# Kernel optimization log

Hardware: AMD Instinct MI355X
Metric: run time of the kernel (lower is better)

## Reference

```python
import jax, jax.numpy as jnp
import numpy as np

B, L, D = 4, 2048, 1024
MD = D // 4      # memory_dim = dim // 4
K = 5            # kernel_size
DIL = 1          # dilation
EPS = 1e-6


def rmsnorm(x, w):
    return w * x * jax.lax.rsqrt(jnp.mean(x * x, axis=-1, keepdims=True) + EPS)


def setup_inputs() -> dict:
    key = jax.random.key(0)
    ks = jax.random.split(key, 16)
    n = lambda k, shape, s=0.02: jax.random.normal(k, shape, jnp.float32) * s
    return dict(
        x=jax.random.normal(ks[0], (B, L, D), jnp.float32),
        memory_state=jnp.zeros((B, MD), jnp.float32),
        norm_w=jnp.ones((D,), jnp.float32),
        dw_kernel=n(ks[1], (D, 1, K), 0.1),   # depthwise conv [O,I/g,K]
        dw_bias=jnp.zeros((D,), jnp.float32),
        pw_kernel=n(ks[2], (D, D)),           # 1x1 conv as [out,in]
        pw_bias=jnp.zeros((D,), jnp.float32),
        Win_w=n(ks[3], (MD, D)), Win_b=jnp.zeros((MD,), jnp.float32),
        Wf_w=n(ks[4], (MD, D + MD)), Wf_b=jnp.ones((MD,), jnp.float32),  # forget bias init 1.0
        Wu_w=n(ks[5], (MD, D + MD)), Wu_b=jnp.zeros((MD,), jnp.float32),
        Wo_w=n(ks[6], (D, D + MD)), Wo_b=jnp.zeros((D,), jnp.float32),
        router_w=n(ks[7], (2, D)), router_b=jnp.zeros((2,), jnp.float32),
        e0_w1=n(ks[8], (D, D)), e0_b1=jnp.zeros((D,), jnp.float32),
        e0_w2=n(ks[9], (D, D)), e0_b2=jnp.zeros((D,), jnp.float32),
        e1_w1=n(ks[10], (D, D)), e1_b1=jnp.zeros((D,), jnp.float32),
        e1_w2=n(ks[11], (D, D)), e1_b2=jnp.zeros((D,), jnp.float32),
        fnorm_w=jnp.ones((D,), jnp.float32),
        down_w=n(ks[12], (D // 4, D)), down_b=jnp.zeros((D // 4,), jnp.float32),
        up_w=n(ks[13], (D, D // 4)), up_b=jnp.zeros((D,), jnp.float32),
    )


def reference(x, memory_state, norm_w, dw_kernel, dw_bias, pw_kernel, pw_bias,
              Win_w, Win_b, Wf_w, Wf_b, Wu_w, Wu_b, Wo_w, Wo_b,
              router_w, router_b, e0_w1, e0_b1, e0_w2, e0_b2,
              e1_w1, e1_b1, e1_w2, e1_b2, fnorm_w, down_w, down_b, up_w, up_b):
    resid = x
    xn = rmsnorm(x, norm_w)                              # [B,L,D]

    # --- causal depthwise conv (left pad (K-1)*DIL == torch pad-both + slice[:L]) + pointwise ---
    P = (K - 1) * DIL
    xc = jnp.swapaxes(xn, 1, 2)                          # [B,D,L]
    xc = jax.lax.conv_general_dilated(
        xc, dw_kernel, window_strides=(1,), padding=[(P, 0)],
        rhs_dilation=(DIL,), dimension_numbers=('NCH', 'OIH', 'NCH'),
        feature_group_count=D) + dw_bias[None, :, None]
    x_conv = jnp.einsum('bdl,ed->ble', xc, pw_kernel) + pw_bias  # [B,L,D]

    # --- structured state recurrence (gated, scan over time) ---
    Wf_x, Wf_m = Wf_w[:, :D], Wf_w[:, D:]
    Wu_x, Wu_m = Wu_w[:, :D], Wu_w[:, D:]
    Wo_x, Wo_m = Wo_w[:, :D], Wo_w[:, D:]
    # precompute all x-dependent projections: [L,B,*]
    fx = jnp.einsum('bld,md->lbm', xn, Wf_x) + Wf_b
    ux = jnp.einsum('bld,md->lbm', xn, Wu_x) + Wu_b
    ox = jnp.einsum('bld,ed->lbe', xn, Wo_x) + Wo_b
    xm = jax.nn.silu(jnp.einsum('bld,md->lbm', xn, Win_w) + Win_b)
    xt = jnp.swapaxes(xn, 0, 1)                          # [L,B,D]

    def step(m, inp):
        fx_t, ux_t, ox_t, xm_t, x_t = inp
        f = jax.nn.sigmoid(fx_t + m @ Wf_m.T)
        u = jax.nn.sigmoid(ux_t + m @ Wu_m.T)
        m2 = f * m + u * xm_t
        out = x_t + ox_t + m2 @ Wo_m.T
        return m2, out

    new_mem, rec = jax.lax.scan(step, memory_state, (fx, ux, ox, xm, xt))
    x_rec = jnp.swapaxes(rec, 0, 1)                      # [B,L,D]

    y = x_conv + x_rec

    # --- enhanced gated fusion (2-expert soft MoE) ---
    r = jax.nn.softmax(y @ router_w.T + router_b, axis=-1)   # [B,L,2]
    e0 = jax.nn.silu(y @ e0_w1.T + e0_b1) @ e0_w2.T + e0_b2
    e1 = jax.nn.silu(y @ e1_w1.T + e1_b1) @ e1_w2.T + e1_b2
    y = rmsnorm(y + r[..., 0:1] * e0 + r[..., 1:2] * e1, fnorm_w)

    # --- low-rank FF (exact GELU) + residual ---
    ff = jax.nn.gelu(y @ down_w.T + down_b, approximate=False) @ up_w.T + up_b
    out = y + ff + resid
    return out, new_mem
```

## Files before the change

kernel.cpp:

```cpp
#include <hip/hip_runtime.h>
#include <hip/hip_bf16.h>

#define DD 1024
#define MDD 256
#define LL 2048
#define BB 4
#define NROWS (BB*LL)

typedef short bf16x8 __attribute__((ext_vector_type(8)));
typedef float f32x4 __attribute__((ext_vector_type(4)));

__device__ __forceinline__ short f2b(float x){
  __hip_bfloat16 h = __float2bfloat16(x);
  return *reinterpret_cast<short*>(&h);
}
__device__ __forceinline__ float b2f(short s){
  return __uint_as_float(((unsigned)(unsigned short)s) << 16);
}
__device__ __forceinline__ float frcp(float x){
#if __has_builtin(__builtin_amdgcn_rcpf)
  return __builtin_amdgcn_rcpf(x);
#else
  float r; asm("v_rcp_f32 %0, %1" : "=v"(r) : "v"(x)); return r;
#endif
}
__device__ __forceinline__ float fsigmoid(float x){
  return frcp(1.f + __expf(-x));
}
__device__ __forceinline__ float sel4(f32x4 a, int kg){
  float lo = (kg & 1) ? a[1] : a[0];
  float hi = (kg & 1) ? a[3] : a[2];
  return (kg & 2) ? hi : lo;
}

__global__ void cvt_submat(const float* __restrict__ src, short* __restrict__ dst,
                           int rows, int cols, int src_ld, int src_off, int dst_ld){
  int n = rows*cols;
  for (int i = blockIdx.x*blockDim.x + threadIdx.x; i < n; i += gridDim.x*blockDim.x){
    int r = i / cols, c = i - r*cols;
    dst[(size_t)r*dst_ld + c] = f2b(src[(size_t)r*src_ld + src_off + c]);
  }
}

__global__ void concat3(const float* __restrict__ a, int na,
                        const float* __restrict__ b, int nb,
                        const float* __restrict__ c, int nc,
                        float* __restrict__ dst){
  int i = blockIdx.x*blockDim.x + threadIdx.x;
  if (i < na) dst[i] = a[i];
  else if (i < na+nb) dst[i] = b[i-na];
  else if (i < na+nb+nc) dst[i] = c[i-na-nb];
}

__global__ void addvec_k(const float* __restrict__ a, const float* __restrict__ b,
                         float* __restrict__ dst, int n){
  int i = blockIdx.x*blockDim.x + threadIdx.x;
  if (i < n) dst[i] = a[i] + b[i];
}

__global__ __launch_bounds__(256) void rmsnorm_k(const float* __restrict__ x,
                                                 const float* __restrict__ w,
                                                 short* __restrict__ xn){
  int row = blockIdx.x, tid = threadIdx.x;
  const float* xr = x + (size_t)row*DD;
  float4 v = *(const float4*)&xr[tid*4];
  float ss = v.x*v.x + v.y*v.y + v.z*v.z + v.w*v.w;
  __shared__ float red[256];
  red[tid] = ss; __syncthreads();
  for (int s = 128; s > 0; s >>= 1){ if (tid < s) red[tid] += red[tid+s]; __syncthreads(); }
  float scale = rsqrtf(red[0]/(float)DD + 1e-6f);
  const float* wr = w + tid*4;
  short4 o;
  o.x = f2b(v.x*wr[0]*scale); o.y = f2b(v.y*wr[1]*scale);
  o.z = f2b(v.z*wr[2]*scale); o.w = f2b(v.w*wr[3]*scale);
  *(short4*)&xn[(size_t)row*2048 + tid*4] = o;
}

__global__ __launch_bounds__(256) void dwconv_k(const short* __restrict__ xnA,
                                                const float* __restrict__ dwk,
                                                const float* __restrict__ dwb,
                                                short* __restrict__ xcA){
  size_t i = (size_t)blockIdx.x*256 + threadIdx.x;
  int d = (int)(i & (DD-1));
  int l = (int)((i >> 10) & (LL-1));
  int b = (int)(i >> 21);
  float acc = dwb[d];
  const float* kk = dwk + d*5;
  #pragma unroll
  for (int k = 0; k < 5; ++k){
    int ll = l + k - 4;
    if (ll >= 0) acc += b2f(xnA[((size_t)(b*LL + ll))*2048 + d]) * kk[k];
  }
  xcA[((size_t)(b*LL + l))*2048 + 1024 + d] = f2b(acc);
}

template<int ACT, int OUTMODE, int PERMUTE>
__global__ __launch_bounds__(256) void gemm_bt(
    const short* __restrict__ A, const short* __restrict__ Bw,
    const float* __restrict__ bias, const float* __restrict__ add0,
    void* __restrict__ Cout, short* __restrict__ Cout2,
    int M, int N, int K, int lda, int nbn){
  __shared__ __align__(16) short As[128*32];
  __shared__ __align__(16) short Bs[128*32];
  int bm = blockIdx.x / nbn, bn = blockIdx.x % nbn;
  int tid = threadIdx.x, lane = tid & 63, w = tid >> 6;
  int wm = (w >> 1)*64, wn = (w & 1)*64;
  const int r0 = lane & 15, kg = lane >> 4;

  f32x4 acc[4][4];
  #pragma unroll
  for (int i = 0; i < 4; ++i)
    #pragma unroll
    for (int j = 0; j < 4; ++j)
      #pragma unroll
      for (int r = 0; r < 4; ++r) acc[i][j][r] = 0.f;

  const int c0 = w*64 + lane;
  const int c1 = c0 + 256;
  const short* a0 = &A [(size_t)(bm*128 + (c0 >> 2))*lda + (c0 & 3)*8];
  const short* a1 = &A [(size_t)(bm*128 + (c1 >> 2))*lda + (c1 & 3)*8];
  const short* b0 = &Bw[(size_t)(bn*128 + (c0 >> 2))*K + (c0 & 3)*8];
  const short* b1 = &Bw[(size_t)(bn*128 + (c1 >> 2))*K + (c1 & 3)*8];

  for (int k0 = 0; k0 < K; k0 += 32){
    __builtin_amdgcn_global_load_lds((const __attribute__((address_space(1))) void*)(a0 + k0),
                                     (__attribute__((address_space(3))) void*)&As[w*512], 16, 0, 0);
    __builtin_amdgcn_global_load_lds((const __attribute__((address_space(1))) void*)(b0 + k0),
                                     (__attribute__((address_space(3))) void*)&Bs[w*512], 16, 0, 0);
    __builtin_amdgcn_global_load_lds((const __attribute__((address_space(1))) void*)(a1 + k0),
                                     (__attribute__((address_space(3))) void*)&As[2048 + w*512], 16, 0, 0);
    __builtin_amdgcn_global_load_lds((const __attribute__((address_space(1))) void*)(b1 + k0),
                                     (__attribute__((address_space(3))) void*)&Bs[2048 + w*512], 16, 0, 0);
    __syncthreads();
    bf16x8 av[4], bv[4];
    #pragma unroll
    for (int i = 0; i < 4; ++i) av[i] = *(const bf16x8*)&As[(wm + i*16 + r0)*32 + kg*8];
    #pragma unroll
    for (int j = 0; j < 4; ++j) bv[j] = *(const bf16x8*)&Bs[(wn + j*16 + r0)*32 + kg*8];
    #pragma unroll
    for (int i = 0; i < 4; ++i)
      #pragma unroll
      for (int j = 0; j < 4; ++j)
        acc[i][j] = __builtin_amdgcn_mfma_f32_16x16x32_bf16(av[i], bv[j], acc[i][j], 0, 0, 0);
    __syncthreads();
  }

  #pragma unroll
  for (int i = 0; i < 4; ++i){
    int grb = bm*128 + wm + i*16 + kg*4;
    #pragma unroll
    for (int j = 0; j < 4; ++j){
      int gc = bn*128 + wn + j*16 + r0;
      float bvv = bias ? bias[gc] : 0.f;
      #pragma unroll
      for (int r = 0; r < 4; ++r){
        int gr = grb + r;
        float v = acc[i][j][r] + bvv;
        if (ACT == 1) v = v / (1.f + __expf(-v));
        else if (ACT == 2) v = 0.5f*v*(1.f + erff(v*0.70710678118f));
        size_t orow = PERMUTE ? (size_t)((gr & 3)*LL + (gr >> 2)) : (size_t)gr;
        size_t oi = orow*(size_t)N + gc;
        if (add0) v += add0[oi];
        if (OUTMODE == 0) ((float*)Cout)[oi] = v;
        else if (OUTMODE == 1) ((float*)Cout)[oi] += v;
        else if (OUTMODE == 2) ((short*)Cout)[oi] = f2b(v);
        else {
          float nv = ((float*)Cout)[oi] + v;
          ((float*)Cout)[oi] = nv;
          Cout2[oi] = f2b(nv);
        }
      }
    }
  }
}

__global__ __launch_bounds__(512) void scan_k(
    const float* __restrict__ fxu, const short* __restrict__ Wfu,
    const float* __restrict__ m0, short* __restrict__ m2all,
    float* __restrict__ newmem){
  __shared__ __align__(16) short mA[2][4*272];
  const int tid = threadIdx.x, lane = tid & 63, w = tid >> 6;
  const int r0 = lane & 15, kg = lane >> 4;
  const int j0 = w*32 + r0;

  bf16x8 bw[2][2][8];
  #pragma unroll
  for (int fu = 0; fu < 2; ++fu)
    #pragma unroll
    for (int p = 0; p < 2; ++p)
      #pragma unroll
      for (int kt = 0; kt < 8; ++kt)
        bw[fu][p][kt] = *(const bf16x8*)&Wfu[(size_t)(fu*256 + w*32 + p*16 + r0)*256 + kt*32 + kg*8];

  float m_reg0 = m0[kg*256 + j0];
  float m_reg1 = m0[kg*256 + j0 + 16];

  float pf_f0, pf_f1, pf_u0, pf_u1, pf_x0, pf_x1;
  {
    size_t base = (size_t)kg*LL*768;
    pf_f0 = fxu[base + j0];        pf_f1 = fxu[base + j0 + 16];
    pf_u0 = fxu[base + 256 + j0];  pf_u1 = fxu[base + 256 + j0 + 16];
    pf_x0 = fxu[base + 512 + j0];  pf_x1 = fxu[base + 512 + j0 + 16];
  }
  mA[0][kg*272 + j0]      = f2b(m_reg0);
  mA[0][kg*272 + j0 + 16] = f2b(m_reg1);
  __syncthreads();

  for (int t = 0; t < LL; ++t){
    const short* mac = mA[t & 1];
    short*       man = mA[(t & 1) ^ 1];

    bf16x8 af[8];
    #pragma unroll
    for (int kt = 0; kt < 8; ++kt)
      af[kt] = *(const bf16x8*)&mac[(r0 & 3)*272 + kt*32 + kg*8];

    f32x4 aF0 = {0.f,0.f,0.f,0.f}, aF1 = {0.f,0.f,0.f,0.f};
    f32x4 aU0 = {0.f,0.f,0.f,0.f}, aU1 = {0.f,0.f,0.f,0.f};
    #pragma unroll
    for (int kt = 0; kt < 8; ++kt){
      aF0 = __builtin_amdgcn_mfma_f32_16x16x32_bf16(af[kt], bw[0][0][kt], aF0, 0, 0, 0);
      aF1 = __builtin_amdgcn_mfma_f32_16x16x32_bf16(af[kt], bw[0][1][kt], aF1, 0, 0, 0);
      aU0 = __builtin_amdgcn_mfma_f32_16x16x32_bf16(af[kt], bw[1][0][kt], aU0, 0, 0, 0);
      aU1 = __builtin_amdgcn_mfma_f32_16x16x32_bf16(af[kt], bw[1][1][kt], aU1, 0, 0, 0);
    }

    float gF0 = sel4(aF0, kg), gF1 = sel4(aF1, kg);
    float gU0 = sel4(aU0, kg), gU1 = sel4(aU1, kg);

    float f0 = fsigmoid(gF0 + pf_f0);
    float f1 = fsigmoid(gF1 + pf_f1);
    float u0 = fsigmoid(gU0 + pf_u0);
    float u1 = fsigmoid(gU1 + pf_u1);
    float xm0 = pf_x0 * fsigmoid(pf_x0);
    float xm1 = pf_x1 * fsigmoid(pf_x1);
    m_reg0 = f0*m_reg0 + u0*xm0;
    m_reg1 = f1*m_reg1 + u1*xm1;
    short mb0 = f2b(m_reg0), mb1 = f2b(m_reg1);

    m2all[(size_t)(t*4 + kg)*256 + j0]      = mb0;
    m2all[(size_t)(t*4 + kg)*256 + j0 + 16] = mb1;

    int t1 = (t + 1 < LL) ? t + 1 : t;
    size_t base = ((size_t)kg*LL + t1)*768;
    pf_f0 = fxu[base + j0];        pf_f1 = fxu[base + j0 + 16];
    pf_u0 = fxu[base + 256 + j0];  pf_u1 = fxu[base + 256 + j0 + 16];
    pf_x0 = fxu[base + 512 + j0];  pf_x1 = fxu[base + 512 + j0 + 16];

    man[kg*272 + j0]      = mb0;
    man[kg*272 + j0 + 16] = mb1;
    asm volatile("s_waitcnt lgkmcnt(0)" ::: "memory");
    __builtin_amdgcn_sched_barrier(0);
    __builtin_amdgcn_s_barrier();
    __builtin_amdgcn_sched_barrier(0);
  }

  newmem[kg*256 + j0]      = m_reg0;
  newmem[kg*256 + j0 + 16] = m_reg1;
}

__global__ __launch_bounds__(256) void combine_k(
    float* __restrict__ y, const short* __restrict__ e0, const short* __restrict__ e1,
    const float* __restrict__ rw, const float* __restrict__ rb,
    const float* __restrict__ fw, short* __restrict__ y2bf){
  int row = blockIdx.x, tid = threadIdx.x;
  size_t base = (size_t)row*DD + tid*4;
  float4 vy = *(const float4*)&y[base];
  short4 s0 = *(const short4*)&e0[base];
  short4 s1 = *(const short4*)&e1[base];
  float4 w0 = *(const float4*)&rw[tid*4];
  float4 w1 = *(const float4*)&rw[DD + tid*4];
  float d0 = vy.x*w0.x + vy.y*w0.y + vy.z*w0.z + vy.w*w0.w;
  float d1 = vy.x*w1.x + vy.y*w1.y + vy.z*w1.z + vy.w*w1.w;
  __shared__ float redA[256], redB[256];
  redA[tid] = d0; redB[tid] = d1; __syncthreads();
  for (int s = 128; s > 0; s >>= 1){
    if (tid < s){ redA[tid] += redA[tid+s]; redB[tid] += redB[tid+s]; }
    __syncthreads();
  }
  float l0 = redA[0] + rb[0], l1 = redB[0] + rb[1];
  float p0 = 1.f/(1.f + __expf(l1 - l0));
  float p1 = 1.f - p0;
  float c0 = vy.x + p0*b2f(s0.x) + p1*b2f(s1.x);
  float c1 = vy.y + p0*b2f(s0.y) + p1*b2f(s1.y);
  float c2 = vy.z + p0*b2f(s0.z) + p1*b2f(s1.z);
  float c3 = vy.w + p0*b2f(s0.w) + p1*b2f(s1.w);
  float ss = c0*c0 + c1*c1 + c2*c2 + c3*c3;
  __syncthreads();
  redA[tid] = ss; __syncthreads();
  for (int s = 128; s > 0; s >>= 1){
    if (tid < s) redA[tid] += redA[tid+s];
    __syncthreads();
  }
  float scale = rsqrtf(redA[0]/(float)DD + 1e-6f);
  const float* fwp = fw + tid*4;
  float o0 = c0*fwp[0]*scale, o1 = c1*fwp[1]*scale, o2 = c2*fwp[2]*scale, o3 = c3*fwp[3]*scale;
  float4 ov; ov.x = o0; ov.y = o1; ov.z = o2; ov.w = o3;
  *(float4*)&y[base] = ov;
  short4 ob; ob.x = f2b(o0); ob.y = f2b(o1); ob.z = f2b(o2); ob.w = f2b(o3);
  *(short4*)&y2bf[base] = ob;
}

extern "C" void kernel_launch(void* const* d_in, const int* in_sizes, int n_in,
                              void* d_out, int out_size, void* d_ws, size_t ws_size,
                              hipStream_t stream){
  (void)in_sizes; (void)n_in; (void)out_size; (void)ws_size;
  const float* x     = (const float*)d_in[0];
  const float* mem0  = (const float*)d_in[1];
  const float* normw = (const float*)d_in[2];
  const float* dwk   = (const float*)d_in[3];
  const float* dwb   = (const float*)d_in[4];
  const float* pw    = (const float*)d_in[5];
  const float* pwb   = (const float*)d_in[6];
  const float* Win_w = (const float*)d_in[7];
  const float* Win_b = (const float*)d_in[8];
  const float* Wf_w  = (const float*)d_in[9];
  const float* Wf_b  = (const float*)d_in[10];
  const float* Wu_w  = (const float*)d_in[11];
  const float* Wu_b  = (const float*)d_in[12];
  const float* Wo_w  = (const float*)d_in[13];
  const float* Wo_b  = (const float*)d_in[14];
  const float* rw    = (const float*)d_in[15];
  const float* rb    = (const float*)d_in[16];
  const float* e0w1  = (const float*)d_in[17];
  const float* e0b1  = (const float*)d_in[18];
  const float* e0w2  = (const float*)d_in[19];
  const float* e0b2  = (const float*)d_in[20];
  const float* e1w1  = (const float*)d_in[21];
  const float* e1b1  = (const float*)d_in[22];
  const float* e1w2  = (const float*)d_in[23];
  const float* e1b2  = (const float*)d_in[24];
  const float* fnw   = (const float*)d_in[25];
  const float* dnw   = (const float*)d_in[26];
  const float* dnb   = (const float*)d_in[27];
  const float* upw   = (const float*)d_in[28];
  const float* upb   = (const float*)d_in[29];

  char* ws = (char*)d_ws;
  size_t off = 0;
  auto alloc = [&](size_t bytes)->char*{
    char* p = ws + off; off += (bytes + 255) & ~(size_t)255; return p;
  };
  short* A2       = (short*)alloc((size_t)NROWS*2048*2);
  short* B2       = (short*)alloc((size_t)1024*2048*2);
  short* W_fxuwin = (short*)alloc((size_t)768*1024*2);
  short* W_fum    = (short*)alloc((size_t)512*256*2);
  short* W_om     = (short*)alloc((size_t)1024*256*2);
  short* W_e0w1   = (short*)alloc((size_t)1024*1024*2);
  short* W_e0w2   = (short*)alloc((size_t)1024*1024*2);
  short* W_e1w1   = (short*)alloc((size_t)1024*1024*2);
  short* W_e1w2   = (short*)alloc((size_t)1024*1024*2);
  short* W_down   = (short*)alloc((size_t)256*1024*2);
  short* W_up     = (short*)alloc((size_t)1024*256*2);
  float* bias768  = (float*)alloc(768*4);
  float* bias2    = (float*)alloc(1024*4);
  float* fxu      = (float*)alloc((size_t)NROWS*768*4);
  float* ybuf     = (float*)alloc((size_t)NROWS*DD*4);
  short* m2all    = (short*)alloc((size_t)NROWS*MDD*2);
  short* ybf      = (short*)alloc((size_t)NROWS*DD*2);
  short* e0v      = (short*)alloc((size_t)NROWS*DD*2);
  short* e1v      = (short*)alloc((size_t)NROWS*DD*2);
  short* h0       = (short*)alloc((size_t)NROWS*DD*2);
  short* h1       = (short*)alloc((size_t)NROWS*DD*2);
  short* hd = m2all;
  short* y2bf = ybf;
  float* y2   = ybuf;

  auto cvt = [&](const float* s, short* d, int rows, int cols, int ld, int o, int dld){
    int n = rows*cols;
    int blocks = (n + 255)/256; if (blocks > 4096) blocks = 4096;
    cvt_submat<<<blocks, 256, 0, stream>>>(s, d, rows, cols, ld, o, dld);
  };
  cvt(Wo_w, B2,                1024, 1024, 1280, 0,    2048);
  cvt(pw,   B2+1024,           1024, 1024, 1024, 0,    2048);
  cvt(Wf_w, W_fxuwin,           256, 1024, 1280, 0,    1024);
  cvt(Wu_w, W_fxuwin+256*1024,  256, 1024, 1280, 0,    1024);
  cvt(Win_w,W_fxuwin+512*1024,  256, 1024, 1024, 0,    1024);
  cvt(Wf_w, W_fum,              256,  256, 1280, 1024, 256);
  cvt(Wu_w, W_fum+256*256,      256,  256, 1280, 1024, 256);
  cvt(Wo_w, W_om,              1024,  256, 1280, 1024, 256);
  cvt(e0w1, W_e0w1,            1024, 1024, 1024, 0,    1024);
  cvt(e0w2, W_e0w2,            1024, 1024, 1024, 0,    1024);
  cvt(e1w1, W_e1w1,            1024, 1024, 1024, 0,    1024);
  cvt(e1w2, W_e1w2,            1024, 1024, 1024, 0,    1024);
  cvt(dnw,  W_down,             256, 1024, 1024, 0,    1024);
  cvt(upw,  W_up,              1024,  256,  256, 0,    256);
  concat3<<<3, 256, 0, stream>>>(Wf_b, 256, Wu_b, 256, Win_b, 256, bias768);
  addvec_k<<<4, 256, 0, stream>>>(Wo_b, pwb, bias2, 1024);

  rmsnorm_k<<<NROWS, 256, 0, stream>>>(x, normw, A2);
  dwconv_k<<<(NROWS*DD)/256, 256, 0, stream>>>(A2, dwk, dwb, A2);

  gemm_bt<0,0,0><<<64*6, 256, 0, stream>>>(A2, W_fxuwin, bias768, nullptr,
                                           fxu, nullptr, NROWS, 768, 1024, 2048, 6);
  gemm_bt<0,0,0><<<64*8, 256, 0, stream>>>(A2, B2, bias2, x,
                                           ybuf, nullptr, NROWS, 1024, 2048, 2048, 8);
  scan_k<<<1, 512, 0, stream>>>(fxu, W_fum, mem0, m2all,
                                (float*)d_out + (size_t)NROWS*DD);
  gemm_bt<0,3,1><<<64*8, 256, 0, stream>>>(m2all, W_om, nullptr, nullptr,
                                           ybuf, ybf, NROWS, 1024, 256, 256, 8);
  gemm_bt<1,2,0><<<64*8, 256, 0, stream>>>(ybf, W_e0w1, e0b1, nullptr,
                                           h0, nullptr, NROWS, 1024, 1024, 1024, 8);
  gemm_bt<1,2,0><<<64*8, 256, 0, stream>>>(ybf, W_e1w1, e1b1, nullptr,
                                           h1, nullptr, NROWS, 1024, 1024, 1024, 8);
  gemm_bt<0,2,0><<<64*8, 256, 0, stream>>>(h0, W_e0w2, e0b2, nullptr,
                                           e0v, nullptr, NROWS, 1024, 1024, 1024, 8);
  gemm_bt<0,2,0><<<64*8, 256, 0, stream>>>(h1, W_e1w2, e1b2, nullptr,
                                           e1v, nullptr, NROWS, 1024, 1024, 1024, 8);
  combine_k<<<NROWS, 256, 0, stream>>>(ybuf, e0v, e1v, rw, rb, fnw, y2bf);
  gemm_bt<2,2,0><<<64*2, 256, 0, stream>>>(y2bf, W_down, dnb, nullptr,
                                           hd, nullptr, NROWS, 256, 1024, 1024, 2);
  gemm_bt<0,0,0><<<64*8, 256, 0, stream>>>(hd, W_up, upb, y2,
                                           (float*)d_out, nullptr, NROWS, 1024, 256, 256, 8);
  addvec_k<<<(NROWS*DD+255)/256, 256, 0, stream>>>((const float*)d_out, x,
                                                   (float*)d_out, NROWS*DD);
}
```

Measured before the change: 2.095 ms.

## Overlap scan with big GEMM, fuse expert up-projections, batch weight conversions

The single-block recurrent scan now launches with 512 extra blocks that compute the conv+output-projection GEMM, so the latency-bound scan overlaps useful matmul work. The two expert first-layer GEMMs are merged into one wider GEMM over concatenated weights. All weight and bias conversions go into a single descriptor-driven kernel, and the final residual add is folded into the up-projection epilogue. The scan also prefetches the silu input two steps ahead and raises wave priority around its MFMAs. The GEMM blocks sharing the launch may contend with the scan block for CU resources.

```diff
diff --git a/kernel.cpp b/kernel.cpp
--- a/kernel.cpp
+++ b/kernel.cpp
@@ -33,29 +33,23 @@
   return (kg & 2) ? hi : lo;
 }
 
-__global__ void cvt_submat(const float* __restrict__ src, short* __restrict__ dst,
-                           int rows, int cols, int src_ld, int src_off, int dst_ld){
-  int n = rows*cols;
-  for (int i = blockIdx.x*blockDim.x + threadIdx.x; i < n; i += gridDim.x*blockDim.x){
-    int r = i / cols, c = i - r*cols;
-    dst[(size_t)r*dst_ld + c] = f2b(src[(size_t)r*src_ld + src_off + c]);
-  }
-}
-
-__global__ void concat3(const float* __restrict__ a, int na,
-                        const float* __restrict__ b, int nb,
-                        const float* __restrict__ c, int nc,
-                        float* __restrict__ dst){
-  int i = blockIdx.x*blockDim.x + threadIdx.x;
-  if (i < na) dst[i] = a[i];
-  else if (i < na+nb) dst[i] = b[i-na];
-  else if (i < na+nb+nc) dst[i] = c[i-na-nb];
-}
-
-__global__ void addvec_k(const float* __restrict__ a, const float* __restrict__ b,
-                         float* __restrict__ dst, int n){
-  int i = blockIdx.x*blockDim.x + threadIdx.x;
-  if (i < n) dst[i] = a[i] + b[i];
+struct CvtDesc {
+  const float* src; const float* src2; short* dstb; float* dstf;
+  int n, cols, sld, soff, dld, mode;
+};
+struct CvtArgs { CvtDesc d[20]; };
+
+__global__ __launch_bounds__(256) void cvt_all(CvtArgs a){
+  int di = blockIdx.x >> 6;
+  CvtDesc d = a.d[di];
+  int base = (blockIdx.x & 63)*256 + threadIdx.x;
+  for (int i = base; i < d.n; i += 64*256){
+    int r = i / d.cols, c = i - r*d.cols;
+    float v = d.src[(size_t)r*d.sld + d.soff + c];
+    if (d.mode == 2) v += d.src2[i];
+    if (d.mode == 0) d.dstb[(size_t)r*d.dld + c] = f2b(v);
+    else             d.dstf[i] = v;
+  }
 }
 
 __global__ __launch_bounds__(256) void rmsnorm_k(const float* __restrict__ x,
@@ -98,8 +92,8 @@
 __global__ __launch_bounds__(256) void gemm_bt(
     const short* __restrict__ A, const short* __restrict__ Bw,
     const float* __restrict__ bias, const float* __restrict__ add0,
-    void* __restrict__ Cout, short* __restrict__ Cout2,
-    int M, int N, int K, int lda, int nbn){
+    const float* __restrict__ add1, void* __restrict__ Cout, short* __restrict__ Cout2,
+    int M, int N, int K, int lda, int ldb, int nbn){
   __shared__ __align__(16) short As[128*32];
   __shared__ __align__(16) short Bs[128*32];
   int bm = blockIdx.x / nbn, bn = blockIdx.x % nbn;
@@ -119,8 +113,8 @@
   const int c1 = c0 + 256;
   const short* a0 = &A [(size_t)(bm*128 + (c0 >> 2))*lda + (c0 & 3)*8];
   const short* a1 = &A [(size_t)(bm*128 + (c1 >> 2))*lda + (c1 & 3)*8];
-  const short* b0 = &Bw[(size_t)(bn*128 + (c0 >> 2))*K + (c0 & 3)*8];
-  const short* b1 = &Bw[(size_t)(bn*128 + (c1 >> 2))*K + (c1 & 3)*8];
+  const short* b0 = &Bw[(size_t)(bn*128 + (c0 >> 2))*ldb + (c0 & 3)*8];
+  const short* b1 = &Bw[(size_t)(bn*128 + (c1 >> 2))*ldb + (c1 & 3)*8];
 
   for (int k0 = 0; k0 < K; k0 += 32){
     __builtin_amdgcn_global_load_lds((const __attribute__((address_space(1))) void*)(a0 + k0),
@@ -161,6 +155,7 @@
         size_t orow = PERMUTE ? (size_t)((gr & 3)*LL + (gr >> 2)) : (size_t)gr;
         size_t oi = orow*(size_t)N + gc;
         if (add0) v += add0[oi];
+        if (add1) v += add1[oi];
         if (OUTMODE == 0) ((float*)Cout)[oi] = v;
         else if (OUTMODE == 1) ((float*)Cout)[oi] += v;
         else if (OUTMODE == 2) ((short*)Cout)[oi] = f2b(v);
@@ -174,13 +169,71 @@
   }
 }
 
-__global__ __launch_bounds__(512) void scan_k(
+__global__ __launch_bounds__(512) void scan_g34_k(
     const float* __restrict__ fxu, const short* __restrict__ Wfu,
-    const float* __restrict__ m0, short* __restrict__ m2all,
-    float* __restrict__ newmem){
-  __shared__ __align__(16) short mA[2][4*272];
+    const float* __restrict__ m0, short* __restrict__ m2all, float* __restrict__ newmem,
+    const short* __restrict__ A2, const short* __restrict__ B2,
+    const float* __restrict__ bias2, const float* __restrict__ xres,
+    float* __restrict__ ybuf){
+  __shared__ __align__(16) short lds[8192];
   const int tid = threadIdx.x, lane = tid & 63, w = tid >> 6;
   const int r0 = lane & 15, kg = lane >> 4;
+
+  if (blockIdx.x != 0){
+    int bid = (int)blockIdx.x - 1;
+    int bm = bid >> 3, bn = bid & 7;
+    short* As = lds;
+    short* Bs = lds + 4096;
+    int wm = (w >> 2)*64, wn = (w & 3)*32;
+    f32x4 acc[4][2];
+    #pragma unroll
+    for (int i = 0; i < 4; ++i)
+      #pragma unroll
+      for (int j = 0; j < 2; ++j)
+        #pragma unroll
+        for (int r = 0; r < 4; ++r) acc[i][j][r] = 0.f;
+
+    const int c = tid;
+    const short* ag = &A2[(size_t)(bm*128 + (c >> 2))*2048 + (c & 3)*8];
+    const short* bg = &B2[(size_t)(bn*128 + (c >> 2))*2048 + (c & 3)*8];
+
+    for (int k0 = 0; k0 < 2048; k0 += 32){
+      __builtin_amdgcn_global_load_lds((const __attribute__((address_space(1))) void*)(ag + k0),
+                                       (__attribute__((address_space(3))) void*)&As[w*512], 16, 0, 0);
+      __builtin_amdgcn_global_load_lds((const __attribute__((address_space(1))) void*)(bg + k0),
+                                       (__attribute__((address_space(3))) void*)&Bs[w*512], 16, 0, 0);
+      __syncthreads();
+      bf16x8 av[4], bv[2];
+      #pragma unroll
+      for (int i = 0; i < 4; ++i) av[i] = *(const bf16x8*)&As[(wm + i*16 + r0)*32 + kg*8];
+      #pragma unroll
+      for (int j = 0; j < 2; ++j) bv[j] = *(const bf16x8*)&Bs[(wn + j*16 + r0)*32 + kg*8];
+      #pragma unroll
+      for (int i = 0; i < 4; ++i)
+        #pragma unroll
+        for (int j = 0; j < 2; ++j)
+          acc[i][j] = __builtin_amdgcn_mfma_f32_16x16x32_bf16(av[i], bv[j], acc[i][j], 0, 0, 0);
+      __syncthreads();
+    }
+    #pragma unroll
+    for (int i = 0; i < 4; ++i){
+      int grb = bm*128 + wm + i*16 + kg*4;
+      #pragma unroll
+      for (int j = 0; j < 2; ++j){
+        int gc = bn*128 + wn + j*16 + r0;
+        float bvv = bias2[gc];
+        #pragma unroll
+        for (int r = 0; r < 4; ++r){
+          size_t oi = (size_t)(grb + r)*1024 + gc;
+          ybuf[oi] = acc[i][j][r] + bvv + xres[oi];
+        }
+      }
+    }
+    return;
+  }
+
+  short* mA0 = lds;
+  short* mA1 = lds + 1088;
   const int j0 = w*32 + r0;
 
   bf16x8 bw[2][2][8];
@@ -195,26 +248,33 @@
   float m_reg0 = m0[kg*256 + j0];
   float m_reg1 = m0[kg*256 + j0 + 16];
 
-  float pf_f0, pf_f1, pf_u0, pf_u1, pf_x0, pf_x1;
+  float cf0, cf1, cu0, cu1, xmc0, xmc1, nx0, nx1;
   {
-    size_t base = (size_t)kg*LL*768;
-    pf_f0 = fxu[base + j0];        pf_f1 = fxu[base + j0 + 16];
-    pf_u0 = fxu[base + 256 + j0];  pf_u1 = fxu[base + 256 + j0 + 16];
-    pf_x0 = fxu[base + 512 + j0];  pf_x1 = fxu[base + 512 + j0 + 16];
-  }
-  mA[0][kg*272 + j0]      = f2b(m_reg0);
-  mA[0][kg*272 + j0 + 16] = f2b(m_reg1);
+    size_t b0 = (size_t)kg*LL*768;
+    cf0 = fxu[b0 + j0];        cf1 = fxu[b0 + j0 + 16];
+    cu0 = fxu[b0 + 256 + j0];  cu1 = fxu[b0 + 256 + j0 + 16];
+    float tx0 = fxu[b0 + 512 + j0], tx1 = fxu[b0 + 512 + j0 + 16];
+    xmc0 = tx0*fsigmoid(tx0);  xmc1 = tx1*fsigmoid(tx1);
+    size_t b1 = b0 + 768;
+    nx0 = fxu[b1 + 512 + j0];  nx1 = fxu[b1 + 512 + j0 + 16];
+  }
+  mA0[kg*272 + j0]      = f2b(m_reg0);
+  mA0[kg*272 + j0 + 16] = f2b(m_reg1);
   __syncthreads();
 
   for (int t = 0; t < LL; ++t){
-    const short* mac = mA[t & 1];
-    short*       man = mA[(t & 1) ^ 1];
+    const short* mac = (t & 1) ? mA1 : mA0;
+    short*       man = (t & 1) ? mA0 : mA1;
 
     bf16x8 af[8];
     #pragma unroll
     for (int kt = 0; kt < 8; ++kt)
       af[kt] = *(const bf16x8*)&mac[(r0 & 3)*272 + kt*32 + kg*8];
 
+    float xmn0 = nx0*fsigmoid(nx0);
+    float xmn1 = nx1*fsigmoid(nx1);
+
+    __builtin_amdgcn_s_setprio(1);
     f32x4 aF0 = {0.f,0.f,0.f,0.f}, aF1 = {0.f,0.f,0.f,0.f};
     f32x4 aU0 = {0.f,0.f,0.f,0.f}, aU1 = {0.f,0.f,0.f,0.f};
     #pragma unroll
@@ -224,28 +284,30 @@
       aU0 = __builtin_amdgcn_mfma_f32_16x16x32_bf16(af[kt], bw[1][0][kt], aU0, 0, 0, 0);
       aU1 = __builtin_amdgcn_mfma_f32_16x16x32_bf16(af[kt], bw[1][1][kt], aU1, 0, 0, 0);
     }
+    __builtin_amdgcn_s_setprio(0);
 
     float gF0 = sel4(aF0, kg), gF1 = sel4(aF1, kg);
     float gU0 = sel4(aU0, kg), gU1 = sel4(aU1, kg);
 
-    float f0 = fsigmoid(gF0 + pf_f0);
-    float f1 = fsigmoid(gF1 + pf_f1);
-    float u0 = fsigmoid(gU0 + pf_u0);
-    float u1 = fsigmoid(gU1 + pf_u1);
-    float xm0 = pf_x0 * fsigmoid(pf_x0);
-    float xm1 = pf_x1 * fsigmoid(pf_x1);
-    m_reg0 = f0*m_reg0 + u0*xm0;
-    m_reg1 = f1*m_reg1 + u1*xm1;
+    float f0 = fsigmoid(gF0 + cf0);
+    float f1 = fsigmoid(gF1 + cf1);
+    float u0 = fsigmoid(gU0 + cu0);
+    float u1 = fsigmoid(gU1 + cu1);
+    m_reg0 = f0*m_reg0 + u0*xmc0;
+    m_reg1 = f1*m_reg1 + u1*xmc1;
     short mb0 = f2b(m_reg0), mb1 = f2b(m_reg1);
 
     m2all[(size_t)(t*4 + kg)*256 + j0]      = mb0;
     m2all[(size_t)(t*4 + kg)*256 + j0 + 16] = mb1;
 
+    xmc0 = xmn0; xmc1 = xmn1;
     int t1 = (t + 1 < LL) ? t + 1 : t;
-    size_t base = ((size_t)kg*LL + t1)*768;
-    pf_f0 = fxu[base + j0];        pf_f1 = fxu[base + j0 + 16];
-    pf_u0 = fxu[base + 256 + j0];  pf_u1 = fxu[base + 256 + j0 + 16];
-    pf_x0 = fxu[base + 512 + j0];  pf_x1 = fxu[base + 512 + j0 + 16];
+    int t2 = (t + 2 < LL) ? t + 2 : t;
+    size_t bfu = ((size_t)kg*LL + t1)*768;
+    size_t bx  = ((size_t)kg*LL + t2)*768;
+    cf0 = fxu[bfu + j0];        cf1 = fxu[bfu + j0 + 16];
+    cu0 = fxu[bfu + 256 + j0];  cu1 = fxu[bfu + 256 + j0 + 16];
+    nx0 = fxu[bx + 512 + j0];   nx1 = fxu[bx + 512 + j0 + 16];
 
     man[kg*272 + j0]      = mb0;
     man[kg*272 + j0 + 16] = mb1;
@@ -346,72 +408,73 @@
   short* W_fxuwin = (short*)alloc((size_t)768*1024*2);
   short* W_fum    = (short*)alloc((size_t)512*256*2);
   short* W_om     = (short*)alloc((size_t)1024*256*2);
-  short* W_e0w1   = (short*)alloc((size_t)1024*1024*2);
+  short* W_e01    = (short*)alloc((size_t)2048*1024*2);
   short* W_e0w2   = (short*)alloc((size_t)1024*1024*2);
-  short* W_e1w1   = (short*)alloc((size_t)1024*1024*2);
   short* W_e1w2   = (short*)alloc((size_t)1024*1024*2);
   short* W_down   = (short*)alloc((size_t)256*1024*2);
   short* W_up     = (short*)alloc((size_t)1024*256*2);
   float* bias768  = (float*)alloc(768*4);
   float* bias2    = (float*)alloc(1024*4);
+  float* bias01   = (float*)alloc(2048*4);
   float* fxu      = (float*)alloc((size_t)NROWS*768*4);
   float* ybuf     = (float*)alloc((size_t)NROWS*DD*4);
   short* m2all    = (short*)alloc((size_t)NROWS*MDD*2);
   short* ybf      = (short*)alloc((size_t)NROWS*DD*2);
   short* e0v      = (short*)alloc((size_t)NROWS*DD*2);
   short* e1v      = (short*)alloc((size_t)NROWS*DD*2);
-  short* h0       = (short*)alloc((size_t)NROWS*DD*2);
-  short* h1       = (short*)alloc((size_t)NROWS*DD*2);
+  short* h01      = (short*)alloc((size_t)NROWS*2048*2);
   short* hd = m2all;
   short* y2bf = ybf;
   float* y2   = ybuf;
 
-  auto cvt = [&](const float* s, short* d, int rows, int cols, int ld, int o, int dld){
-    int n = rows*cols;
-    int blocks = (n + 255)/256; if (blocks > 4096) blocks = 4096;
-    cvt_submat<<<blocks, 256, 0, stream>>>(s, d, rows, cols, ld, o, dld);
+  CvtArgs ca;
+  auto D0 = [&](const float* s, short* db, int rows, int cols, int sld, int soff, int dld){
+    return CvtDesc{s, nullptr, db, nullptr, rows*cols, cols, sld, soff, dld, 0};
   };
-  cvt(Wo_w, B2,                1024, 1024, 1280, 0,    2048);
-  cvt(pw,   B2+1024,           1024, 1024, 1024, 0,    2048);
-  cvt(Wf_w, W_fxuwin,           256, 1024, 1280, 0,    1024);
-  cvt(Wu_w, W_fxuwin+256*1024,  256, 1024, 1280, 0,    1024);
-  cvt(Win_w,W_fxuwin+512*1024,  256, 1024, 1024, 0,    1024);
-  cvt(Wf_w, W_fum,              256,  256, 1280, 1024, 256);
-  cvt(Wu_w, W_fum+256*256,      256,  256, 1280, 1024, 256);
-  cvt(Wo_w, W_om,              1024,  256, 1280, 1024, 256);
-  cvt(e0w1, W_e0w1,            1024, 1024, 1024, 0,    1024);
-  cvt(e0w2, W_e0w2,            1024, 1024, 1024, 0,    1024);
-  cvt(e1w1, W_e1w1,            1024, 1024, 1024, 0,    1024);
-  cvt(e1w2, W_e1w2,            1024, 1024, 1024, 0,    1024);
-  cvt(dnw,  W_down,             256, 1024, 1024, 0,    1024);
-  cvt(upw,  W_up,              1024,  256,  256, 0,    256);
-  concat3<<<3, 256, 0, stream>>>(Wf_b, 256, Wu_b, 256, Win_b, 256, bias768);
-  addvec_k<<<4, 256, 0, stream>>>(Wo_b, pwb, bias2, 1024);
+  auto D1 = [&](const float* s, float* df, int n){
+    return CvtDesc{s, nullptr, nullptr, df, n, n, 0, 0, 0, 1};
+  };
+  ca.d[0]  = D0(Wo_w,  B2,                1024, 1024, 1280, 0,    2048);
+  ca.d[1]  = D0(pw,    B2+1024,           1024, 1024, 1024, 0,    2048);
+  ca.d[2]  = D0(Wf_w,  W_fxuwin,           256, 1024, 1280, 0,    1024);
+  ca.d[3]  = D0(Wu_w,  W_fxuwin+256*1024,  256, 1024, 1280, 0,    1024);
+  ca.d[4]  = D0(Win_w, W_fxuwin+512*1024,  256, 1024, 1024, 0,    1024);
+  ca.d[5]  = D0(Wf_w,  W_fum,              256,  256, 1280, 1024, 256);
+  ca.d[6]  = D0(Wu_w,  W_fum+256*256,      256,  256, 1280, 1024, 256);
+  ca.d[7]  = D0(Wo_w,  W_om,              1024,  256, 1280, 1024, 256);
+  ca.d[8]  = D0(e0w1,  W_e01,             1024, 1024, 1024, 0,    1024);
+  ca.d[9]  = D0(e1w1,  W_e01+1024*1024,   1024, 1024, 1024, 0,    1024);
+  ca.d[10] = D0(e0w2,  W_e0w2,            1024, 1024, 1024, 0,    1024);
+  ca.d[11] = D0(e1w2,  W_e1w2,            1024, 1024, 1024, 0,    1024);
+  ca.d[12] = D0(dnw,   W_down,             256, 1024, 1024, 0,    1024);
+  ca.d[13] = D0(upw,   W_up,              1024,  256,  256, 0,    256);
+  ca.d[14] = D1(Wf_b,  bias768,       256);
+  ca.d[15] = D1(Wu_b,  bias768+256,   256);
+  ca.d[16] = D1(Win_b, bias768+512,   256);
+  ca.d[17] = CvtDesc{Wo_b, pwb, nullptr, bias2, 1024, 1024, 0, 0, 0, 2};
+  ca.d[18] = D1(e0b1,  bias01,       1024);
+  ca.d[19] = D1(e1b1,  bias01+1024,  1024);
+  cvt_all<<<20*64, 256, 0, stream>>>(ca);
 
   rmsnorm_k<<<NROWS, 256, 0, stream>>>(x, normw, A2);
   dwconv_k<<<(NROWS*DD)/256, 256, 0, stream>>>(A2, dwk, dwb, A2);
 
-  gemm_bt<0,0,0><<<64*6, 256, 0, stream>>>(A2, W_fxuwin, bias768, nullptr,
-                                           fxu, nullptr, NROWS, 768, 1024, 2048, 6);
-  gemm_bt<0,0,0><<<64*8, 256, 0, stream>>>(A2, B2, bias2, x,
-                                           ybuf, nullptr, NROWS, 1024, 2048, 2048, 8);
-  scan_k<<<1, 512, 0, stream>>>(fxu, W_fum, mem0, m2all,
-                                (float*)d_out + (size_t)NROWS*DD);
-  gemm_bt<0,3,1><<<64*8, 256, 0, stream>>>(m2all, W_om, nullptr, nullptr,
-                                           ybuf, ybf, NROWS, 1024, 256, 256, 8);
-  gemm_bt<1,2,0><<<64*8, 256, 0, stream>>>(ybf, W_e0w1, e0b1, nullptr,
-                                           h0, nullptr, NROWS, 1024, 1024, 1024, 8);
-  gemm_bt<1,2,0><<<64*8, 256, 0, stream>>>(ybf, W_e1w1, e1b1, nullptr,
-                                           h1, nullptr, NROWS, 1024, 1024, 1024, 8);
-  gemm_bt<0,2,0><<<64*8, 256, 0, stream>>>(h0, W_e0w2, e0b2, nullptr,
-                                           e0v, nullptr, NROWS, 1024, 1024, 1024, 8);
-  gemm_bt<0,2,0><<<64*8, 256, 0, stream>>>(h1, W_e1w2, e1b2, nullptr,
-                                           e1v, nullptr, NROWS, 1024, 1024, 1024, 8);
+  gemm_bt<0,0,0><<<64*6, 256, 0, stream>>>(A2, W_fxuwin, bias768, nullptr, nullptr,
+                                           fxu, nullptr, NROWS, 768, 1024, 2048, 1024, 6);
+  scan_g34_k<<<513, 512, 0, stream>>>(fxu, W_fum, mem0, m2all,
+                                      (float*)d_out + (size_t)NROWS*DD,
+                                      A2, B2, bias2, x, ybuf);
+  gemm_bt<0,3,1><<<64*8, 256, 0, stream>>>(m2all, W_om, nullptr, nullptr, nullptr,
+                                           ybuf, ybf, NROWS, 1024, 256, 256, 256, 8);
+  gemm_bt<1,2,0><<<64*16, 256, 0, stream>>>(ybf, W_e01, bias01, nullptr, nullptr,
+                                            h01, nullptr, NROWS, 2048, 1024, 1024, 1024, 16);
+  gemm_bt<0,2,0><<<64*8, 256, 0, stream>>>(h01, W_e0w2, e0b2, nullptr, nullptr,
+                                           e0v, nullptr, NROWS, 1024, 1024, 2048, 1024, 8);
+  gemm_bt<0,2,0><<<64*8, 256, 0, stream>>>(h01+1024, W_e1w2, e1b2, nullptr, nullptr,
+                                           e1v, nullptr, NROWS, 1024, 1024, 2048, 1024, 8);
   combine_k<<<NROWS, 256, 0, stream>>>(ybuf, e0v, e1v, rw, rb, fnw, y2bf);
-  gemm_bt<2,2,0><<<64*2, 256, 0, stream>>>(y2bf, W_down, dnb, nullptr,
-                                           hd, nullptr, NROWS, 256, 1024, 1024, 2);
-  gemm_bt<0,0,0><<<64*8, 256, 0, stream>>>(hd, W_up, upb, y2,
-                                           (float*)d_out, nullptr, NROWS, 1024, 256, 256, 8);
-  addvec_k<<<(NROWS*DD+255)/256, 256, 0, stream>>>((const float*)d_out, x,
-                                                   (float*)d_out, NROWS*DD);
-}
+  gemm_bt<2,2,0><<<64*2, 256, 0, stream>>>(y2bf, W_down, dnb, nullptr, nullptr,
+                                           hd, nullptr, NROWS, 256, 1024, 1024, 1024, 2);
+  gemm_bt<0,0,0><<<64*8, 256, 0, stream>>>(hd, W_up, upb, y2, x,
+                                           (float*)d_out, nullptr, NROWS, 1024, 256, 256, 256, 8);
+}
```

Result: faster. 1.927 ms (-8.0%).
